# Kernel optimization log

Measured on AMD Instinct MI355X. Metric: run time of the kernel, lower is better.

Reference implementation:

```python
import jax, jax.numpy as jnp
import numpy as np

NUM_POSES = 4096
NUM_PATCHES = 262144
NUM_OBS = 2097152


def setup_inputs() -> dict:
    key = jax.random.key(0)
    ks = jax.random.split(key, 7)
    poses = jax.random.normal(ks[0], (NUM_POSES, 7), dtype=jnp.float32)
    patch_coords = jax.random.normal(ks[1], (NUM_PATCHES, 2), dtype=jnp.float32)
    elevation_angle = jax.random.normal(ks[2], (NUM_PATCHES, 1), dtype=jnp.float32)
    poses_idx = jax.random.randint(ks[3], (NUM_OBS,), 0, NUM_POSES)
    patch_idx = jax.random.randint(ks[4], (NUM_OBS,), 0, NUM_PATCHES)
    target_coords = jax.random.normal(ks[5], (NUM_OBS, 3), dtype=jnp.float32)
    weights = jax.random.uniform(ks[6], (NUM_OBS, 1), dtype=jnp.float32)
    return {
        "poses": poses,
        "patch_coords": patch_coords,
        "elevation_angle": elevation_angle,
        "poses_idx": poses_idx,
        "patch_idx": patch_idx,
        "target_coords": target_coords,
        "weights": weights,
    }


def _se3_apply(pose7, pts):
    # pose7: [M,7] = (tx,ty,tz,qx,qy,qz,qw); pts: [M,3]
    # Equivalent to transform_matrix(pose) @ [pts; 1] (rotation by unit quaternion + translation)
    t = pose7[:, :3]
    q = pose7[:, 3:]
    q = q / jnp.linalg.norm(q, axis=-1, keepdims=True)  # pp.SE3 keeps unit quats
    qv, qw = q[:, :3], q[:, 3:4]
    uv = jnp.cross(qv, pts)                     # [M,3]
    rotated = pts + 2.0 * (qw * uv + jnp.cross(qv, uv))
    return rotated + t


def _cart2polar(xyz):
    # (x,y,z) -> (range, azimuth, elevation)
    x, y, z = xyz[:, 0], xyz[:, 1], xyz[:, 2]
    rho = jnp.sqrt(x * x + y * y)
    r = jnp.sqrt(rho * rho + z * z)
    az = jnp.arctan2(y, x)
    el = jnp.arctan2(z, rho)
    return jnp.stack([r, az, el], axis=1)


def reference(poses, patch_coords, elevation_angle, poses_idx, patch_idx, target_coords, weights):
    p = poses[poses_idx]                                            # [M,7] gather
    pts = jnp.concatenate(
        [patch_coords[patch_idx], elevation_angle[patch_idx]], axis=1
    )                                                               # [M,3] gather+cat
    proj = _cart2polar(_se3_apply(p, pts))                          # [M,3]
    residual = (proj - target_coords) * weights                     # [M,3]
    return residual
```

## Files before the change

### kernel.cpp

```cpp
#include <hip/hip_runtime.h>
#include <hip/hip_bf16.h>


#define NPOSES      4096
#define POSE_DWORDS (NPOSES * 7)
#define POSE_VEC4   (POSE_DWORDS / 4)

typedef float fvec4 __attribute__((ext_vector_type(4)));
typedef int   ivec4 __attribute__((ext_vector_type(4)));

__global__ __launch_bounds__(1024) void ba_one_kernel(
    const float* __restrict__ poses,
    const float* __restrict__ patch_coords,
    const float* __restrict__ elev,
    const int*   __restrict__ poses_idx,
    const int*   __restrict__ patch_idx,
    const float* __restrict__ target,
    const float* __restrict__ weights,
    float*       __restrict__ out,
    int n8)
{
    extern __shared__ float lds[];
    int tid = threadIdx.x;

    {
        const fvec4* src = reinterpret_cast<const fvec4*>(poses);
        fvec4* dst = reinterpret_cast<fvec4*>(lds);
#pragma unroll
        for (int j = 0; j < POSE_VEC4 / 1024; ++j)
            dst[tid + j * 1024] = src[tid + j * 1024];
    }
    __syncthreads();

    int i8 = blockIdx.x * blockDim.x + tid;
    if (i8 >= n8) return;

    const ivec4* pi4 = reinterpret_cast<const ivec4*>(poses_idx);
    const ivec4* qi4 = reinterpret_cast<const ivec4*>(patch_idx);
    const fvec4* w4p = reinterpret_cast<const fvec4*>(weights);
    const fvec4* tg4 = reinterpret_cast<const fvec4*>(target) + (size_t)i8 * 6;
    fvec4*       o4  = reinterpret_cast<fvec4*>(out) + (size_t)i8 * 6;

#pragma unroll
    for (int g = 0; g < 2; ++g) {
        ivec4 pidx = pi4[(size_t)i8 * 2 + g];
        ivec4 qidx = qi4[(size_t)i8 * 2 + g];
        fvec4 w4   = w4p[(size_t)i8 * 2 + g];
        fvec4 t0 = tg4[g * 3 + 0];
        fvec4 t1 = tg4[g * 3 + 1];
        fvec4 t2 = tg4[g * 3 + 2];

        int   pi[4] = {pidx.x, pidx.y, pidx.z, pidx.w};
        int   qi[4] = {qidx.x, qidx.y, qidx.z, qidx.w};
        float ww[4] = {w4.x, w4.y, w4.z, w4.w};
        float tg[12] = {t0.x, t0.y, t0.z, t0.w,
                        t1.x, t1.y, t1.z, t1.w,
                        t2.x, t2.y, t2.z, t2.w};

        float res[12];

#pragma unroll
        for (int k = 0; k < 4; ++k) {
            const float* pl = lds + pi[k] * 7;
            float tx = pl[0], ty = pl[1], tz = pl[2];
            float qx = pl[3], qy = pl[4], qz = pl[5], qw = pl[6];
            float inv = rsqrtf(qx*qx + qy*qy + qz*qz + qw*qw);
            qx *= inv; qy *= inv; qz *= inv; qw *= inv;

            float2 pc = *reinterpret_cast<const float2*>(patch_coords + (size_t)qi[k] * 2);
            float px = pc.x, py = pc.y, pz = elev[qi[k]];

            float ux = qy*pz - qz*py;
            float uy = qz*px - qx*pz;
            float uz = qx*py - qy*px;
            float cx = qy*uz - qz*uy;
            float cy = qz*ux - qx*uz;
            float cz = qx*uy - qy*ux;
            float rx = px + 2.0f*(qw*ux + cx) + tx;
            float ry = py + 2.0f*(qw*uy + cy) + ty;
            float rz = pz + 2.0f*(qw*uz + cz) + tz;

            float rho = sqrtf(rx*rx + ry*ry);
            float r   = sqrtf(rho*rho + rz*rz);
            float az  = atan2f(ry, rx);
            float el  = atan2f(rz, rho);

            res[k*3 + 0] = (r  - tg[k*3 + 0]) * ww[k];
            res[k*3 + 1] = (az - tg[k*3 + 1]) * ww[k];
            res[k*3 + 2] = (el - tg[k*3 + 2]) * ww[k];
        }

        o4[g * 3 + 0] = (fvec4){res[0], res[1], res[2],  res[3]};
        o4[g * 3 + 1] = (fvec4){res[4], res[5], res[6],  res[7]};
        o4[g * 3 + 2] = (fvec4){res[8], res[9], res[10], res[11]};
    }
}

__global__ __launch_bounds__(256) void ba_fallback_kernel(
    const float* __restrict__ poses, const float* __restrict__ patch_coords,
    const float* __restrict__ elev, const int* __restrict__ poses_idx,
    const int* __restrict__ patch_idx, const float* __restrict__ target,
    const float* __restrict__ weights, float* __restrict__ out, int n)
{
    int i = blockIdx.x * blockDim.x + threadIdx.x;
    if (i >= n) return;
    int pi = poses_idx[i];
    int qi = patch_idx[i];
    const float* p = poses + (size_t)pi * 7;
    float tx = p[0], ty = p[1], tz = p[2];
    float qx = p[3], qy = p[4], qz = p[5], qw = p[6];
    float inv = rsqrtf(qx*qx + qy*qy + qz*qz + qw*qw);
    qx *= inv; qy *= inv; qz *= inv; qw *= inv;
    float2 pc = *reinterpret_cast<const float2*>(patch_coords + (size_t)qi * 2);
    float px = pc.x, py = pc.y, pz = elev[qi];
    float ux = qy*pz - qz*py, uy = qz*px - qx*pz, uz = qx*py - qy*px;
    float cx = qy*uz - qz*uy, cy = qz*ux - qx*uz, cz = qx*uy - qy*ux;
    float rx = px + 2.0f*(qw*ux + cx) + tx;
    float ry = py + 2.0f*(qw*uy + cy) + ty;
    float rz = pz + 2.0f*(qw*uz + cz) + tz;
    float rho = sqrtf(rx*rx + ry*ry);
    float r   = sqrtf(rho*rho + rz*rz);
    float az  = atan2f(ry, rx);
    float el  = atan2f(rz, rho);
    float w = weights[i];
    out[(size_t)i*3+0] = (r  - target[(size_t)i*3+0]) * w;
    out[(size_t)i*3+1] = (az - target[(size_t)i*3+1]) * w;
    out[(size_t)i*3+2] = (el - target[(size_t)i*3+2]) * w;
}

extern "C" void kernel_launch(void* const* d_in, const int* in_sizes, int n_in,
                              void* d_out, int out_size, void* d_ws, size_t ws_size,
                              hipStream_t stream) {
    const float* poses        = (const float*)d_in[0];
    const float* patch_coords = (const float*)d_in[1];
    const float* elev         = (const float*)d_in[2];
    const int*   poses_idx    = (const int*)d_in[3];
    const int*   patch_idx    = (const int*)d_in[4];
    const float* target       = (const float*)d_in[5];
    const float* weights      = (const float*)d_in[6];
    float*       out          = (float*)d_out;

    int n  = in_sizes[3];
    int n8 = n / 8;

    size_t lds_bytes = (size_t)POSE_DWORDS * 4;

    hipError_t attr_err = hipFuncSetAttribute(
        reinterpret_cast<const void*>(ba_one_kernel),
        hipFuncAttributeMaxDynamicSharedMemorySize, (int)lds_bytes);

    if (attr_err == hipSuccess) {
        int block = 1024;
        int grid  = (n8 + block - 1) / block;
        ba_one_kernel<<<grid, block, lds_bytes, stream>>>(
            poses, patch_coords, elev, poses_idx, patch_idx,
            target, weights, out, n8);
    } else {
        ba_fallback_kernel<<<(n + 255) / 256, 256, 0, stream>>>(
            poses, patch_coords, elev, poses_idx, patch_idx, target, weights, out, n);
    }
}
```

Baseline: 50.12 us.

## Pre-pack patch and pose tables, use nontemporal streaming loads and stores

Adds a pre-pass kernel that packs each patch (x, y, elevation) into a 16-byte record and stores pre-normalized poses in LDS with a stride of 9. The patch gather becomes one dwordx4 load instead of two scattered loads, and the per-observation quaternion normalization is removed. Streaming inputs and outputs now use nontemporal loads and stores so they do not pollute the cache, and gather loads use sc0. The cost is an extra kernel launch plus a write of the packed table (about 4 MB). A full vmcnt(0) wait with a scheduling barrier also limits overlap, and the LDS footprint grows to about 147 KB, which depends on the 160 KB LDS of MI355.

```diff
diff --git a/kernel.cpp b/kernel.cpp
--- a/kernel.cpp
+++ b/kernel.cpp
@@ -2,17 +2,49 @@
 #include <hip/hip_bf16.h>
 
 
-#define NPOSES      4096
-#define POSE_DWORDS (NPOSES * 7)
-#define POSE_VEC4   (POSE_DWORDS / 4)
+#define NPOSES   4096
+#define NPATCHES 262144
+#define POSE_STRIDE 9
+#define POSE_LDS_FLOATS (NPOSES * POSE_STRIDE)
+#define POSE_LDS_VEC4   (POSE_LDS_FLOATS / 4)
 
 typedef float fvec4 __attribute__((ext_vector_type(4)));
 typedef int   ivec4 __attribute__((ext_vector_type(4)));
 
-__global__ __launch_bounds__(1024) void ba_one_kernel(
+__global__ __launch_bounds__(256) void pack_tables_kernel(
     const float* __restrict__ poses,
     const float* __restrict__ patch_coords,
     const float* __restrict__ elev,
+    float*       __restrict__ pose9,
+    fvec4*       __restrict__ patch4,
+    int n)
+{
+    int i = blockIdx.x * blockDim.x + threadIdx.x;
+    if (i >= n) return;
+    float2 pc = *reinterpret_cast<const float2*>(patch_coords + (size_t)i * 2);
+    patch4[i] = (fvec4){pc.x, pc.y, elev[i], 0.0f};
+
+    if (i < NPOSES) {
+        const float* p = poses + (size_t)i * 7;
+        float tx = p[0], ty = p[1], tz = p[2];
+        float qx = p[3], qy = p[4], qz = p[5], qw = p[6];
+        float inv = rsqrtf(qx*qx + qy*qy + qz*qz + qw*qw);
+        float* d = pose9 + (size_t)i * POSE_STRIDE;
+        d[0] = tx;      d[1] = ty;      d[2] = tz;
+        d[3] = qx*inv;  d[4] = qy*inv;  d[5] = qz*inv;  d[6] = qw*inv;
+        d[7] = 0.0f;    d[8] = 0.0f;
+    }
+}
+
+__device__ __forceinline__ fvec4 load_sc0(const fvec4* addr) {
+    fvec4 v;
+    asm volatile("global_load_dwordx4 %0, %1, off sc0" : "=v"(v) : "v"(addr));
+    return v;
+}
+
+__global__ __launch_bounds__(1024) void ba_main_kernel(
+    const float* __restrict__ pose9,
+    const fvec4* __restrict__ patch4,
     const int*   __restrict__ poses_idx,
     const int*   __restrict__ patch_idx,
     const float* __restrict__ target,
@@ -20,55 +52,60 @@
     float*       __restrict__ out,
     int n8)
 {
-    extern __shared__ float lds[];
+    __shared__ float lds[POSE_LDS_FLOATS];
     int tid = threadIdx.x;
 
     {
-        const fvec4* src = reinterpret_cast<const fvec4*>(poses);
+        const fvec4* src = reinterpret_cast<const fvec4*>(pose9);
         fvec4* dst = reinterpret_cast<fvec4*>(lds);
 #pragma unroll
-        for (int j = 0; j < POSE_VEC4 / 1024; ++j)
-            dst[tid + j * 1024] = src[tid + j * 1024];
+        for (int k = 0; k < POSE_LDS_VEC4 / 1024; ++k)
+            dst[tid + k * 1024] = src[tid + k * 1024];
     }
     __syncthreads();
 
     int i8 = blockIdx.x * blockDim.x + tid;
     if (i8 >= n8) return;
 
-    const ivec4* pi4 = reinterpret_cast<const ivec4*>(poses_idx);
-    const ivec4* qi4 = reinterpret_cast<const ivec4*>(patch_idx);
-    const fvec4* w4p = reinterpret_cast<const fvec4*>(weights);
+    const ivec4* pi4 = reinterpret_cast<const ivec4*>(poses_idx) + (size_t)i8 * 2;
+    const ivec4* qi4 = reinterpret_cast<const ivec4*>(patch_idx) + (size_t)i8 * 2;
+    const fvec4* w4p = reinterpret_cast<const fvec4*>(weights) + (size_t)i8 * 2;
     const fvec4* tg4 = reinterpret_cast<const fvec4*>(target) + (size_t)i8 * 6;
     fvec4*       o4  = reinterpret_cast<fvec4*>(out) + (size_t)i8 * 6;
 
 #pragma unroll
     for (int g = 0; g < 2; ++g) {
-        ivec4 pidx = pi4[(size_t)i8 * 2 + g];
-        ivec4 qidx = qi4[(size_t)i8 * 2 + g];
-        fvec4 w4   = w4p[(size_t)i8 * 2 + g];
-        fvec4 t0 = tg4[g * 3 + 0];
-        fvec4 t1 = tg4[g * 3 + 1];
-        fvec4 t2 = tg4[g * 3 + 2];
+        ivec4 pidx = __builtin_nontemporal_load(pi4 + g);
+        ivec4 qidx = __builtin_nontemporal_load(qi4 + g);
+
+        fvec4 pp0 = load_sc0(patch4 + qidx.x);
+        fvec4 pp1 = load_sc0(patch4 + qidx.y);
+        fvec4 pp2 = load_sc0(patch4 + qidx.z);
+        fvec4 pp3 = load_sc0(patch4 + qidx.w);
+
+        fvec4 w4 = __builtin_nontemporal_load(w4p + g);
+        fvec4 t0 = __builtin_nontemporal_load(tg4 + g * 3 + 0);
+        fvec4 t1 = __builtin_nontemporal_load(tg4 + g * 3 + 1);
+        fvec4 t2 = __builtin_nontemporal_load(tg4 + g * 3 + 2);
+
+        asm volatile("s_waitcnt vmcnt(0)" ::: "memory");
+        __builtin_amdgcn_sched_barrier(0);
 
         int   pi[4] = {pidx.x, pidx.y, pidx.z, pidx.w};
-        int   qi[4] = {qidx.x, qidx.y, qidx.z, qidx.w};
         float ww[4] = {w4.x, w4.y, w4.z, w4.w};
         float tg[12] = {t0.x, t0.y, t0.z, t0.w,
                         t1.x, t1.y, t1.z, t1.w,
                         t2.x, t2.y, t2.z, t2.w};
+        fvec4 pp[4] = {pp0, pp1, pp2, pp3};
 
         float res[12];
-
 #pragma unroll
         for (int k = 0; k < 4; ++k) {
-            const float* pl = lds + pi[k] * 7;
+            const float* pl = lds + pi[k] * POSE_STRIDE;
             float tx = pl[0], ty = pl[1], tz = pl[2];
             float qx = pl[3], qy = pl[4], qz = pl[5], qw = pl[6];
-            float inv = rsqrtf(qx*qx + qy*qy + qz*qz + qw*qw);
-            qx *= inv; qy *= inv; qz *= inv; qw *= inv;
-
-            float2 pc = *reinterpret_cast<const float2*>(patch_coords + (size_t)qi[k] * 2);
-            float px = pc.x, py = pc.y, pz = elev[qi[k]];
+
+            float px = pp[k].x, py = pp[k].y, pz = pp[k].z;
 
             float ux = qy*pz - qz*py;
             float uy = qz*px - qx*pz;
@@ -90,9 +127,9 @@
             res[k*3 + 2] = (el - tg[k*3 + 2]) * ww[k];
         }
 
-        o4[g * 3 + 0] = (fvec4){res[0], res[1], res[2],  res[3]};
-        o4[g * 3 + 1] = (fvec4){res[4], res[5], res[6],  res[7]};
-        o4[g * 3 + 2] = (fvec4){res[8], res[9], res[10], res[11]};
+        __builtin_nontemporal_store((fvec4){res[0], res[1], res[2],  res[3]},  o4 + g*3 + 0);
+        __builtin_nontemporal_store((fvec4){res[4], res[5], res[6],  res[7]},  o4 + g*3 + 1);
+        __builtin_nontemporal_store((fvec4){res[8], res[9], res[10], res[11]}, o4 + g*3 + 2);
     }
 }
 
@@ -143,18 +180,20 @@
     int n  = in_sizes[3];
     int n8 = n / 8;
 
-    size_t lds_bytes = (size_t)POSE_DWORDS * 4;
-
-    hipError_t attr_err = hipFuncSetAttribute(
-        reinterpret_cast<const void*>(ba_one_kernel),
-        hipFuncAttributeMaxDynamicSharedMemorySize, (int)lds_bytes);
-
-    if (attr_err == hipSuccess) {
+    size_t patch_bytes = (size_t)NPATCHES * 16;
+    size_t pose_bytes  = (size_t)POSE_LDS_FLOATS * 4;
+
+    if (ws_size >= patch_bytes + pose_bytes) {
+        fvec4* patch4 = (fvec4*)d_ws;
+        float* pose9  = (float*)((char*)d_ws + patch_bytes);
+
+        pack_tables_kernel<<<(NPATCHES + 255) / 256, 256, 0, stream>>>(
+            poses, patch_coords, elev, pose9, patch4, NPATCHES);
+
         int block = 1024;
         int grid  = (n8 + block - 1) / block;
-        ba_one_kernel<<<grid, block, lds_bytes, stream>>>(
-            poses, patch_coords, elev, poses_idx, patch_idx,
-            target, weights, out, n8);
+        ba_main_kernel<<<grid, block, 0, stream>>>(
+            pose9, patch4, poses_idx, patch_idx, target, weights, out, n8);
     } else {
         ba_fallback_kernel<<<(n + 255) / 256, 256, 0, stream>>>(
             poses, patch_coords, elev, poses_idx, patch_idx, target, weights, out, n);
```

After: 71.94 us. +43.5%, slower.
